# Performance work log

Measured on AMD Instinct MI355X. Metric: run time of the kernel, lower is better.

Reference implementation:

```python
import jax, jax.numpy as jnp
import numpy as np

DIMX, DIMZ, N = 32, 16, 32768
TWO_PI = 2.0 * np.pi

def _sym(M):
    return 0.5 * (M + M.T)

def setup_inputs() -> dict:
    key = jax.random.key(0)
    kx, ka, kc = jax.random.split(key, 3)
    x = jax.random.normal(kx, (DIMX, N), dtype=jnp.float32)
    A = jnp.eye(DIMZ, dtype=jnp.float32) + 0.001 * jax.random.normal(ka, (DIMZ, DIMZ), dtype=jnp.float32)
    C = jax.random.uniform(kc, (DIMX, DIMZ), dtype=jnp.float32)
    Q = 0.01 * jnp.eye(DIMZ, dtype=jnp.float32)
    R = 0.1 * jnp.eye(DIMX, dtype=jnp.float32)
    m0 = jnp.zeros((DIMZ, 1), dtype=jnp.float32)
    P0 = jnp.eye(DIMZ, dtype=jnp.float32)
    Sigma_AQA = 1e-9 * jnp.ones((DIMZ, DIMZ), dtype=jnp.float32)
    Sigma_CRC = 1e-9 * jnp.ones((DIMZ, DIMZ), dtype=jnp.float32)
    return {"x": x, "A": A, "C": C, "Q": Q, "R": R, "m0": m0, "P0": P0,
            "Sigma_AQA": Sigma_AQA, "Sigma_CRC": Sigma_CRC}

def _vblds_forward(x, A, C, Q, R, m0, P0, Sigma_AQA, Sigma_CRC):
    dz = A.shape[0]
    n_steps = x.shape[-1]
    I = jnp.eye(dz, dtype=x.dtype)

    def woodbury(V, S):
        # I - V @ inv(I + S @ V) @ S
        return I - V @ jnp.linalg.inv(I + S @ V) @ S

    # ---------- filter (forward scan over time) ----------
    def filter_step(carry, x_n):
        m, P = carry                       # m: (dz,), P: (dz,dz)
        L = woodbury(P, Sigma_CRC)
        Lm = L @ m
        LP = L @ P
        x_hat = C @ Lm
        S_hat = C @ LP @ C.T + R
        K = LP @ C.T @ jnp.linalg.inv(S_hat)
        mu = Lm + K @ (x_n - x_hat)
        V = _sym((I - K @ C) @ LP)
        # predict
        G = woodbury(V, Sigma_AQA)
        m_next = A @ (G @ mu)
        P_next = _sym(A @ G @ V @ A.T + Q)
        return (m_next, P_next), (mu, V)

    (_, _), (muf, Vf) = jax.lax.scan(filter_step, (m0[:, 0], P0), x.T)
    # muf: (N, dz), Vf: (N, dz, dz)

    # ---------- RTS smoother (reverse scan) ----------
    def smooth_step(carry, inp):
        mu_plus, V_plus = carry
        muf_n, Vf_n = inp
        G = woodbury(Vf_n, Sigma_AQA)
        GV = G @ Vf_n
        m = A @ (G @ muf_n)
        P = _sym(A @ GV @ A.T + Q)
        J = GV @ A.T @ jnp.linalg.inv(P)
        mu = G @ muf_n + J @ (mu_plus - m)
        V = _sym(GV + J @ (V_plus - P) @ J.T)
        V12 = J @ V_plus
        return (mu, V), (mu, V, V12)

    (_, _), (mus_head, Vs_head, V12) = jax.lax.scan(
        smooth_step, (muf[-1], Vf[-1]), (muf[:-1], Vf[:-1]), reverse=True)
    mus = jnp.concatenate([mus_head, muf[-1:]], axis=0)    # (N, dz)
    Vs = jnp.concatenate([Vs_head, Vf[-1:]], axis=0)        # (N, dz, dz)

    # ---------- learn (VB M-step) -> evidence lower bound pieces ----------
    Nf = jnp.asarray(n_steps, dtype=x.dtype)
    zz = jnp.einsum('ni,nj->ij', mus, mus) + Vs.sum(0)
    z1z1 = jnp.einsum('ni,nj->ij', mus[:-1], mus[:-1]) + Vs[:-1].sum(0)
    z1z2 = jnp.einsum('ni,nj->ij', mus[:-1], mus[1:]) + V12.sum(0)
    z2z2 = jnp.einsum('ni,nj->ij', mus[1:], mus[1:]) + Vs[1:].sum(0)
    zx = jnp.einsum('ni,jn->ij', mus, x)                    # (dz, dimx)
    xx = x @ x.T

    # learn_mP (quad reduces to Vs[0] since m0 <- mus[0])
    P0_new = _sym(Vs[0])
    mu0 = mus[0]
    m0m0 = jnp.outer(mu0, mu0)
    z0z0 = m0m0 + Vs[0]
    quad0 = _sym(z0z0 - 2.0 * m0m0 + m0m0)
    ell_z0 = (-0.5 * jnp.linalg.slogdet(TWO_PI * P0_new)[1]
              - 0.5 * jnp.trace(jnp.linalg.solve(P0_new, quad0)))

    # learn_AQ: alpha = 1e-6 ones -> same Lam for every row i
    Sigma_A = jnp.linalg.inv(z1z1 + 1e-6 * I)
    A_new = z1z2.T @ Sigma_A                                 # row i = z1z2[:, i] @ Sigma_A
    c_hat = 1e-9 + 0.5 * (Nf - 1.0)
    d_hat = 1e-9 + 0.5 * (jnp.diag(z2z2) - jnp.einsum('ij,ji->i', A_new, z1z2))
    Q_diag = d_hat / c_hat
    Az1z2 = A_new @ z1z2
    quad_z = _sym(z2z2 - (Az1z2 + Az1z2.T) + A_new @ z1z1 @ A_new.T)
    ell_z = (-(Nf - 1.0) / 2.0 * jnp.sum(jnp.log(TWO_PI * Q_diag))
             - 0.5 * jnp.sum(jnp.diag(quad_z) / Q_diag))

    # learn_CR: beta = 1e-6 ones -> same Lam for every row i
    Sigma_C = jnp.linalg.inv(zz + 1e-6 * I)
    C_new = zx.T @ Sigma_C                                   # (dimx, dz)
    a_hat = 1e-9 + 0.5 * Nf
    b_hat = 1e-9 + 0.5 * (jnp.diag(xx) - jnp.einsum('ij,ji->i', C_new, zx))
    R_diag = b_hat / a_hat
    Czx = C_new @ zx
    quad_x = _sym(xx - (Czx + Czx.T) + C_new @ zz @ C_new.T)
    ell_x = (-Nf / 2.0 * jnp.sum(jnp.log(TWO_PI * R_diag))
             - 0.5 * jnp.sum(jnp.diag(quad_x) / R_diag))

    ell = ell_z + ell_x + ell_z0

    # match original layout: (dz, N) and (dz, dz, N)
    return (ell,
            muf.T, jnp.moveaxis(Vf, 0, -1),
            mus.T, jnp.moveaxis(Vs, 0, -1),
            jnp.moveaxis(V12, 0, -1))

def reference(x, A, C, Q, R, m0, P0, Sigma_AQA, Sigma_CRC):
    return _vblds_forward(x, A, C, Q, R, m0, P0, Sigma_AQA, Sigma_CRC)
```

## Files before the change

### kernel.cpp

```cpp
#include <hip/hip_runtime.h>

#define DZ 16
#define NT 32768
#define NTF 32768.0f
#define NCONV 32
#define NCONVB 32
#define WARM 48
#define CHUNK 32
#define NMIDF 32703.0f
#define TWO_PI_F 6.28318530717958647692f

typedef float f4 __attribute__((ext_vector_type(4)));

#define LD4(A_, r_, c_) (*(const f4*)&(A_)[r_][c_])
#define ST4(A_, r_, c_, v_) (*((f4*)&(A_)[r_][c_])) = (v_)
#define RF(a_, k_) (a_[(k_) >> 2][(k_) & 3])
#define GATH(val_, q_) __shfl((val_), (((j4 + (q_)) << 2) | jg), 64)

template<int CTRL>
__device__ __forceinline__ float dadd(float v) {
    return v + __int_as_float(__builtin_amdgcn_update_dpp(
        0, __float_as_int(v), CTRL, 0xF, 0xF, true));
}
__device__ __forceinline__ float qred(float v) {
    return dadd<0x4E>(dadd<0xB1>(v));
}
__device__ __forceinline__ float wred64(float v) {
    v = dadd<0x128>(dadd<0x124>(dadd<0x4E>(dadd<0xB1>(v))));
    v += __int_as_float(__builtin_amdgcn_ds_swizzle(__float_as_int(v), 0x401F));
    v += __shfl_xor(v, 32, 64);
    return v;
}
template<int C>
__device__ __forceinline__ float qb(float v) {
    return __int_as_float(__builtin_amdgcn_update_dpp(
        0, __float_as_int(v), C | (C << 2) | (C << 4) | (C << 6), 0xF, 0xF, true));
}
__device__ __forceinline__ void qrows(const f4 v, f4 r[4]) {
    #pragma unroll
    for (int q = 0; q < 4; ++q) {
        r[0][q] = qb<0>(v[q]); r[1][q] = qb<1>(v[q]);
        r[2][q] = qb<2>(v[q]); r[3][q] = qb<3>(v[q]);
    }
}
__device__ __forceinline__ float frcp(float x) { return __builtin_amdgcn_rcpf(x); }
__device__ __forceinline__ float sum4(f4 v) { return (v.x + v.y) + (v.z + v.w); }
__device__ __forceinline__ float dot4(f4 a, f4 b) { f4 m = a * b; return (m.x + m.y) + (m.z + m.w); }

template<int EXTRA>
__device__ __forceinline__ void gjreg(f4& m4, f4& r4, float& rex, float& pd, int i, int jg)
{
    pd = 1.0f;
    #pragma unroll
    for (int k = 0; k < 16; ++k) {
        const int kq = k >> 2, kr = k & 3;
        const int lk = (k << 2) | jg;
        float piv = __shfl(m4[kr], (k << 2) | kq, 64);
        float mik = __shfl(m4[kr], (i << 2) | kq, 64);
        f4 mk, rk;
        #pragma unroll
        for (int q = 0; q < 4; ++q) {
            mk[q] = __shfl(m4[q], lk, 64);
            rk[q] = __shfl(r4[q], lk, 64);
        }
        float rexk = EXTRA ? __shfl(rex, lk, 64) : 0.f;
        float f = mik * frcp(piv);
        if (i != k) {
            m4 -= f * mk;
            r4 -= f * rk;
            if (EXTRA) rex -= f * rexk;
        } else {
            pd = piv;
        }
    }
}

template<int EXTRA>
__device__ __forceinline__ void gj16w(float (*M)[20], float (*RHS)[20], int i, int jg, int j4)
{
    for (int k = 0; k < 16; ++k) {
        float piv = M[k][k];
        float f = M[i][k] / piv;
        f4 mk = LD4(M, k, j4);
        f4 rk = LD4(RHS, k, j4);
        float rex = EXTRA ? RHS[k][16] : 0.f;
        f4 mi4 = LD4(M, i, j4);
        f4 ri4 = LD4(RHS, i, j4);
        float rei = (EXTRA && jg == 0) ? RHS[i][16] : 0.f;
        __syncthreads();
        if (i != k) {
            ST4(M, i, j4, mi4 - f * mk);
            ST4(RHS, i, j4, ri4 - f * rk);
            if (EXTRA && jg == 0) RHS[i][16] = rei - f * rex;
        }
        __syncthreads();
    }
}

__device__ __forceinline__ void gj16b(float (*M)[17], float (*RHS)[18], int i, int j)
{
    for (int k = 0; k < 16; ++k) {
        float f = M[i][k] / M[k][k];
        __syncthreads();
        if (i != k) {
            M[i][j]   -= f * M[k][j];
            RHS[i][j] -= f * RHS[k][j];
        }
        __syncthreads();
    }
}

__global__ __launch_bounds__(64) void vblds_phaseA(
    const float* __restrict__ gx,
    const float* __restrict__ gA, const float* __restrict__ gC,
    const float* __restrict__ gQ, const float* __restrict__ gR,
    const float* __restrict__ gm0, const float* __restrict__ gP0,
    const float* __restrict__ gSaqa, const float* __restrict__ gScrc,
    float* __restrict__ gmuf, float* __restrict__ gVf,
    float* __restrict__ gVs, float* __restrict__ gV12,
    float* __restrict__ wss)
{
    __shared__ __align__(16) float sA[16][20], sW[16][20];
    __shared__ __align__(16) float sC[32][20];
    __shared__ __align__(16) float sLP[16][20], sM[16][20], sRHS[16][20];
    __shared__ __align__(16) float sV[16][20], sGV[16][20], sAG[16][20];
    __shared__ __align__(16) float sX[16][20], sT1[16][20], sT2[16][20];
    __shared__ __align__(16) float sPp[16][20], sJm[16][20], sY[16][20], sVp[16][20];
    __shared__ __align__(16) float sKb[16][36];
    __shared__ __align__(16) float sLm[16];
    __shared__ float sRinv[32], sr[32];
    __shared__ float sxA[32][33];

    const int tid = threadIdx.x;
    const int i  = tid >> 2;
    const int jg = tid & 3;
    const int j4 = jg << 2;

    for (int idx = tid; idx < 256; idx += 64) sA[idx >> 4][idx & 15] = gA[idx];
    for (int idx = tid; idx < 512; idx += 64) sC[idx >> 4][idx & 15] = gC[idx];
    if (tid < 32) sRinv[tid] = 1.0f / gR[tid * 32 + tid];
    for (int idx = tid; idx < 32 * NCONV; idx += 64)
        sxA[idx >> 5][idx & 31] = gx[(size_t)(idx >> 5) * NT + (idx & 31)];
    const float crc = gScrc[0], aqa = gSaqa[0];
    float mi = gm0[i];
    f4 pv = *(const f4*)&gP0[i * 16 + j4];
    __syncthreads();

    {
        f4 w = {0.f, 0.f, 0.f, 0.f};
        for (int k = 0; k < 32; ++k) {
            float cri = sC[k][i] * sRinv[k];
            w += cri * LD4(sC, k, j4);
        }
        ST4(sW, i, j4, w);
    }
    __syncthreads();

    f4 ar[4], arj, qv;
    #pragma unroll
    for (int c = 0; c < 4; ++c) ar[c] = LD4(sA, i, c * 4);
    arj = LD4(sA, i, j4);
    qv = *(const f4*)&gQ[i * 16 + j4];

    for (int n = 0; n < NCONV; ++n) {
        float rs = sum4(pv);
        float P1_i = qred(rs);
        float totP = wred64(rs);
        float totm = wred64(mi) * 0.25f;
        float c1 = crc / (1.0f + crc * totP);
        float cm = c1 * totm;
        f4 p1g;
        #pragma unroll
        for (int q = 0; q < 4; ++q) p1g[q] = GATH(P1_i, q);
        f4 lpv = pv - (c1 * P1_i) * p1g;
        float Lm_i = mi - cm * P1_i;
        if (jg == 0) sLm[i] = Lm_i;
        __syncthreads();
        {
            int row = tid >> 1, h = tid & 1;
            f4 ca = LD4(sC, row, h * 8), cb = LD4(sC, row, h * 8 + 4);
            f4 la = *(const f4*)&sLm[h * 8], lb = *(const f4*)&sLm[h * 8 + 4];
            float part = dot4(ca, la) + dot4(cb, lb);
            part = dadd<0xB1>(part);
            if (h == 0) sr[row] = (sxA[row][n] - part) * sRinv[row];
        }
        __syncthreads();
        float b_i;
        {
            float accv = 0.f;
            #pragma unroll
            for (int kk = 0; kk < 8; ++kk) {
                int k = jg * 8 + kk;
                accv += sC[k][i] * sr[k];
            }
            b_i = qred(accv);
        }
        f4 bg;
        #pragma unroll
        for (int q = 0; q < 4; ++q) bg[q] = GATH(b_i, q);
        float LPb_i = qred(dot4(lpv, bg));
        f4 lr[4];
        qrows(lpv, lr);
        f4 m4 = {0.f, 0.f, 0.f, 0.f};
        #pragma unroll
        for (int k = 0; k < 16; ++k) m4 += RF(lr, k) * LD4(sW, k, j4);
        #pragma unroll
        for (int q = 0; q < 4; ++q) if (i == j4 + q) m4[q] += 1.0f;
        f4 r4 = lpv;
        float rex = LPb_i, pd;
        gjreg<1>(m4, r4, rex, pd, i, jg);
        float pdr = frcp(pd);
        f4 vv = r4 * pdr;
        float mu_i = Lm_i + rex * pdr;
        ST4(sV, i, j4, vv);
        __syncthreads();
        f4 vt;
        #pragma unroll
        for (int q = 0; q < 4; ++q) vt[q] = sV[j4 + q][i];
        f4 vs4 = 0.5f * (vv + vt);
        #pragma unroll
        for (int q = 0; q < 4; ++q) gVf[(size_t)(i * 16 + j4 + q) * NT + n] = vs4[q];
        if (jg == 0) gmuf[(size_t)i * NT + n] = mu_i;
        float rsv = sum4(vs4);
        float V1_i = qred(rsv);
        float totV = wred64(rsv);
        float totmu = wred64(mu_i) * 0.25f;
        float c2 = aqa / (1.0f + aqa * totV);
        float cm2 = c2 * totmu;
        f4 v1g;
        #pragma unroll
        for (int q = 0; q < 4; ++q) v1g[q] = GATH(V1_i, q);
        f4 gv4 = vs4 - (c2 * V1_i) * v1g;
        float Gmu_i = mu_i - cm2 * V1_i;
        ST4(sGV, i, j4, gv4);
        __syncthreads();
        f4 ag4 = {0.f, 0.f, 0.f, 0.f};
        #pragma unroll
        for (int k = 0; k < 16; ++k) ag4 += RF(ar, k) * LD4(sGV, k, j4);
        f4 gmug;
        #pragma unroll
        for (int q = 0; q < 4; ++q) gmug[q] = GATH(Gmu_i, q);
        float mv_i = qred(dot4(arj, gmug));
        f4 agr[4];
        qrows(ag4, agr);
        f4 pn;
        #pragma unroll
        for (int q = 0; q < 4; ++q) {
            f4 acc4 = {0.f, 0.f, 0.f, 0.f};
            #pragma unroll
            for (int c = 0; c < 4; ++c) acc4 += agr[c] * LD4(sA, j4 + q, c * 4);
            pn[q] = qv[q] + sum4(acc4);
        }
        ST4(sM, i, j4, pn);
        __syncthreads();
        f4 pt;
        #pragma unroll
        for (int q = 0; q < 4; ++q) pt[q] = sM[j4 + q][i];
        pv = 0.5f * (pn + pt);
        mi = mv_i;
    }
    __syncthreads();

    f4 vss4, gvs4;
    f4 jmr[4];
    {
        float rs = sum4(pv);
        float P1_i = qred(rs);
        float totP = wred64(rs);
        float c1 = crc / (1.0f + crc * totP);
        f4 p1g;
        #pragma unroll
        for (int q = 0; q < 4; ++q) p1g[q] = GATH(P1_i, q);
        f4 lpv = pv - (c1 * P1_i) * p1g;
        ST4(sLP, i, j4, lpv);
        __syncthreads();
        {
            f4 lr[4];
            #pragma unroll
            for (int c = 0; c < 4; ++c) lr[c] = LD4(sLP, i, c * 4);
            f4 m4 = {0.f, 0.f, 0.f, 0.f};
            #pragma unroll
            for (int k = 0; k < 16; ++k) m4 += RF(lr, k) * LD4(sW, k, j4);
            #pragma unroll
            for (int q = 0; q < 4; ++q) if (i == j4 + q) m4[q] += 1.0f;
            ST4(sM, i, j4, m4);
            ST4(sRHS, i, j4, lpv);
        }
        __syncthreads();
        gj16w<0>(sM, sRHS, i, jg, j4);
        float pd = sM[i][i];
        f4 xv = LD4(sRHS, i, j4) / pd;
        ST4(sX, i, j4, xv);
        __syncthreads();
        f4 xt;
        #pragma unroll
        for (int q = 0; q < 4; ++q) xt[q] = sX[j4 + q][i];
        vss4 = 0.5f * (xv + xt);
        #pragma unroll
        for (int q = 0; q < 4; ++q) {
            wss[2048 + i * 16 + j4 + q] = vss4[q];
            gVs[(size_t)(i * 16 + j4 + q) * NT + (NT - 1)] = vss4[q];
        }
        f4 xr[4];
        #pragma unroll
        for (int c = 0; c < 4; ++c) xr[c] = LD4(sX, i, c * 4);
        f4 t4 = {0.f, 0.f, 0.f, 0.f};
        #pragma unroll
        for (int k = 0; k < 16; ++k) t4 -= RF(xr, k) * LD4(sW, k, j4);
        #pragma unroll
        for (int q = 0; q < 4; ++q) if (i == j4 + q) t4[q] += 1.0f;
        float tp1_i = qred(dot4(t4, p1g));
        f4 u4 = t4 - c1 * tp1_i;
        #pragma unroll
        for (int q = 0; q < 4; ++q) wss[768 + i * 16 + j4 + q] = u4[q];
        ST4(sT1, i, j4, u4);
        f4 k0, k1;
        #pragma unroll
        for (int q = 0; q < 4; ++q) {
            int c = j4 + q;
            k0[q] = (dot4(xr[0], LD4(sC, c, 0)) + dot4(xr[1], LD4(sC, c, 4))
                   + dot4(xr[2], LD4(sC, c, 8)) + dot4(xr[3], LD4(sC, c, 12))) * sRinv[c];
            int c2 = c + 16;
            k1[q] = (dot4(xr[0], LD4(sC, c2, 0)) + dot4(xr[1], LD4(sC, c2, 4))
                   + dot4(xr[2], LD4(sC, c2, 8)) + dot4(xr[3], LD4(sC, c2, 12))) * sRinv[c2];
        }
        #pragma unroll
        for (int q = 0; q < 4; ++q) {
            sKb[i][j4 + q] = k0[q]; sKb[i][j4 + 16 + q] = k1[q];
            wss[1024 + i * 32 + j4 + q] = k0[q];
            wss[1024 + i * 32 + 16 + j4 + q] = k1[q];
        }
        __syncthreads();
        float rsv = sum4(vss4);
        float v1_i = qred(rsv);
        float totV = wred64(rsv);
        float cA = aqa / (1.0f + aqa * totV);
        f4 v1g;
        #pragma unroll
        for (int q = 0; q < 4; ++q) v1g[q] = GATH(v1_i, q);
        float av_i = qred(dot4(arj, v1g));
        f4 agm4 = arj - cA * av_i;
        gvs4 = vss4 - (cA * v1_i) * v1g;
        ST4(sAG, i, j4, agm4);
        ST4(sGV, i, j4, gvs4);
        __syncthreads();
        f4 agmr[4];
        #pragma unroll
        for (int c = 0; c < 4; ++c) agmr[c] = LD4(sAG, i, c * 4);
        f4 fv = {0.f, 0.f, 0.f, 0.f}, b0 = {0.f, 0.f, 0.f, 0.f}, b1 = {0.f, 0.f, 0.f, 0.f};
        #pragma unroll
        for (int k = 0; k < 16; ++k) {
            float a = RF(agmr, k);
            fv += a * LD4(sT1, k, j4);
            b0 += a * LD4(sKb, k, j4);
            b1 += a * LD4(sKb, k, j4 + 16);
        }
        #pragma unroll
        for (int q = 0; q < 4; ++q) {
            wss[0 + i * 16 + j4 + q] = fv[q];
            wss[256 + i * 32 + j4 + q] = b0[q];
            wss[256 + i * 32 + 16 + j4 + q] = b1[q];
        }
        f4 t2 = {0.f, 0.f, 0.f, 0.f};
        #pragma unroll
        for (int k = 0; k < 16; ++k) t2 += RF(ar, k) * LD4(sGV, k, j4);
        ST4(sT2, i, j4, t2);
        __syncthreads();
        f4 t2r[4];
        #pragma unroll
        for (int c = 0; c < 4; ++c) t2r[c] = LD4(sT2, i, c * 4);
        f4 pp;
        #pragma unroll
        for (int q = 0; q < 4; ++q) {
            f4 acc4 = {0.f, 0.f, 0.f, 0.f};
            #pragma unroll
            for (int c = 0; c < 4; ++c) acc4 += t2r[c] * LD4(sA, j4 + q, c * 4);
            pp[q] = qv[q] + sum4(acc4);
        }
        ST4(sM, i, j4, pp);
        __syncthreads();
        f4 ppt;
        #pragma unroll
        for (int q = 0; q < 4; ++q) ppt[q] = sM[j4 + q][i];
        f4 pp4 = 0.5f * (pp + ppt);
        ST4(sPp, i, j4, pp4);
        ST4(sM, i, j4, pp4);
        ST4(sRHS, i, j4, t2);
        __syncthreads();
        gj16w<0>(sM, sRHS, i, jg, j4);
        float pd2 = sM[i][i];
        f4 yv = LD4(sRHS, i, j4) / pd2;
        ST4(sY, i, j4, yv);
        __syncthreads();
        f4 jm4;
        #pragma unroll
        for (int q = 0; q < 4; ++q) jm4[q] = sY[j4 + q][i];
        ST4(sJm, i, j4, jm4);
        #pragma unroll
        for (int q = 0; q < 4; ++q) wss[1536 + i * 16 + j4 + q] = jm4[q];
        __syncthreads();
        #pragma unroll
        for (int c = 0; c < 4; ++c) jmr[c] = LD4(sJm, i, c * 4);
        f4 s4 = {0.f, 0.f, 0.f, 0.f};
        #pragma unroll
        for (int k = 0; k < 16; ++k) s4 -= RF(jmr, k) * LD4(sA, k, j4);
        #pragma unroll
        for (int q = 0; q < 4; ++q) if (i == j4 + q) s4[q] += 1.0f;
        float sv_i = qred(dot4(s4, v1g));
        f4 S4 = s4 - cA * sv_i;
        #pragma unroll
        for (int q = 0; q < 4; ++q) wss[1792 + i * 16 + j4 + q] = S4[q];
        ST4(sVp, i, j4, vss4);
        __syncthreads();
    }

    for (int k2 = 1; k2 <= NCONVB; ++k2) {
        int n = NT - 1 - k2;
        f4 v12 = {0.f, 0.f, 0.f, 0.f}, t14 = {0.f, 0.f, 0.f, 0.f};
        #pragma unroll
        for (int k = 0; k < 16; ++k) {
            f4 vp = LD4(sVp, k, j4);
            float jik = RF(jmr, k);
            v12 += jik * vp;
            t14 += jik * (vp - LD4(sPp, k, j4));
        }
        #pragma unroll
        for (int q = 0; q < 4; ++q) gV12[(size_t)(i * 16 + j4 + q) * (NT - 1) + n] = v12[q];
        f4 t1r[4];
        qrows(t14, t1r);
        f4 vn;
        #pragma unroll
        for (int q = 0; q < 4; ++q) {
            f4 acc4 = {0.f, 0.f, 0.f, 0.f};
            #pragma unroll
            for (int c = 0; c < 4; ++c) acc4 += t1r[c] * LD4(sJm, j4 + q, c * 4);
            vn[q] = gvs4[q] + sum4(acc4);
        }
        ST4(sT2, i, j4, vn);
        __syncthreads();
        f4 vnt;
        #pragma unroll
        for (int q = 0; q < 4; ++q) vnt[q] = sT2[j4 + q][i];
        f4 vnew = 0.5f * (vn + vnt);
        ST4(sVp, i, j4, vnew);
        #pragma unroll
        for (int q = 0; q < 4; ++q) gVs[(size_t)(i * 16 + j4 + q) * NT + n] = vnew[q];
        __syncthreads();
    }
    {
        f4 vpf = LD4(sVp, i, j4);
        #pragma unroll
        for (int q = 0; q < 4; ++q) wss[2304 + i * 16 + j4 + q] = vpf[q];
        f4 v12ss = {0.f, 0.f, 0.f, 0.f};
        #pragma unroll
        for (int k = 0; k < 16; ++k) v12ss += RF(jmr, k) * LD4(sVp, k, j4);
        #pragma unroll
        for (int q = 0; q < 4; ++q) wss[2560 + i * 16 + j4 + q] = v12ss[q];
    }
}

__global__ __launch_bounds__(64) void vblds_muf_scan(
    const float* __restrict__ gx, const float* __restrict__ wss, float* __restrict__ gmuf)
{
    __shared__ __align__(16) float sx[CHUNK + WARM][36];
    const int c = blockIdx.x, tid = threadIdx.x;
    const int i = tid >> 2, jg = tid & 3, j4 = jg << 2;
    const int n0 = NCONV + c * CHUNK;
    const int CLc = (NT - n0 < CHUNK) ? (NT - n0) : CHUNK;
    const int wlen = (c == 0) ? NCONV : WARM;
    const int w0 = n0 - wlen;
    const int T = wlen + CLc;

    const f4 Fv  = *(const f4*)&wss[0 + i * 16 + j4];
    const f4 Uv  = *(const f4*)&wss[768 + i * 16 + j4];
    const f4 Bh0 = *(const f4*)&wss[256 + i * 32 + jg * 8];
    const f4 Bh1 = *(const f4*)&wss[256 + i * 32 + jg * 8 + 4];
    const f4 Kh0 = *(const f4*)&wss[1024 + i * 32 + jg * 8];
    const f4 Kh1 = *(const f4*)&wss[1024 + i * 32 + jg * 8 + 4];

    for (int r = 0; r < 32; ++r)
        for (int t = tid; t < T; t += 64)
            sx[t][r] = gx[(size_t)r * NT + w0 + t];
    __syncthreads();

    float m = 0.f;
    for (int t = 0; t < T; ++t) {
        f4 mg;
        #pragma unroll
        for (int q = 0; q < 4; ++q) mg[q] = __shfl(m, ((j4 + q) << 2) | jg, 64);
        f4 xa = *(const f4*)&sx[t][jg * 8];
        f4 xb = *(const f4*)&sx[t][jg * 8 + 4];
        float pm = dot4(Fv, mg) + dot4(Bh0, xa) + dot4(Bh1, xb);
        float po = dot4(Uv, mg) + dot4(Kh0, xa) + dot4(Kh1, xb);
        pm = qred(pm);
        po = qred(po);
        if (t >= wlen && jg == 0) gmuf[(size_t)i * NT + w0 + t] = po;
        m = pm;
    }
}

__global__ __launch_bounds__(64) void vblds_mus_scan(
    const float* __restrict__ gmuf, const float* __restrict__ wss, float* __restrict__ gmus)
{
    __shared__ __align__(16) float smu[CHUNK + WARM][20];
    const int c = blockIdx.x, tid = threadIdx.x;
    const int i = tid >> 2, jg = tid & 3, j4 = jg << 2;
    const int n0 = NCONV + c * CHUNK;
    const int CLc = (NT - n0 < CHUNK) ? (NT - n0) : CHUNK;
    int wend = n0 + CLc - 1 + WARM;
    int exact = 0;
    if (wend >= NT - 1) { wend = NT - 1; exact = 1; }
    const int T = wend - n0 + 1;

    const f4 Jv = *(const f4*)&wss[1536 + i * 16 + j4];
    const f4 Sv = *(const f4*)&wss[1792 + i * 16 + j4];

    for (int r = 0; r < 16; ++r)
        for (int t = tid; t < T; t += 64)
            smu[t][r] = gmuf[(size_t)r * NT + n0 + t];
    __syncthreads();

    float cst;
    int tstart;
    if (exact) {
        cst = smu[T - 1][i];
        if (T - 1 < CLc && jg == 0) gmus[(size_t)i * NT + n0 + T - 1] = cst;
        tstart = T - 2;
    } else {
        cst = 0.f;
        tstart = T - 1;
    }
    for (int t = tstart; t >= 0; --t) {
        f4 cg;
        #pragma unroll
        for (int q = 0; q < 4; ++q) cg[q] = __shfl(cst, ((j4 + q) << 2) | jg, 64);
        f4 mufv = *(const f4*)&smu[t][j4];
        float p = dot4(Sv, mufv) + dot4(Jv, cg);
        p = qred(p);
        if (t < CLc && jg == 0) gmus[(size_t)i * NT + n0 + t] = p;
        cst = p;
    }
}

__global__ __launch_bounds__(64) void vblds_phaseB(
    const float* __restrict__ gA, const float* __restrict__ gQ,
    const float* __restrict__ gSaqa,
    const float* __restrict__ gmuf, const float* __restrict__ gVf,
    float* __restrict__ gmus, float* __restrict__ gVs, float* __restrict__ gV12,
    const float* __restrict__ wss)
{
    __shared__ __align__(16) float sA[16][20];
    __shared__ __align__(16) float sGV[16][20], sM[16][20];
    __shared__ __align__(16) float sPm[16][20], sY[16][20], sVp[16][20], sT2[16][20];
    const int tid = threadIdx.x;
    const int i = tid >> 2, jg = tid & 3, j4 = jg << 2;

    for (int idx = tid; idx < 256; idx += 64) sA[idx >> 4][idx & 15] = gA[idx];
    const float aqa = gSaqa[0];
    {
        f4 vp = *(const f4*)&wss[2304 + i * 16 + j4];
        ST4(sVp, i, j4, vp);
    }
    float mup_i = gmus[(size_t)i * NT + NCONV];
    __syncthreads();
    f4 ar[4], arj, qv;
    #pragma unroll
    for (int c = 0; c < 4; ++c) ar[c] = LD4(sA, i, c * 4);
    arj = LD4(sA, i, j4);
    qv = *(const f4*)&gQ[i * 16 + j4];

    f4 vfc;
    #pragma unroll
    for (int q = 0; q < 4; ++q) vfc[q] = gVf[(size_t)(i * 16 + j4 + q) * NT + (NCONV - 1)];
    float mfc = gmuf[(size_t)i * NT + (NCONV - 1)];

    for (int n = NCONV - 1; n >= 0; --n) {
        f4 vfn = vfc; float mfn = mfc;
        if (n > 0) {
            #pragma unroll
            for (int q = 0; q < 4; ++q) vfn[q] = gVf[(size_t)(i * 16 + j4 + q) * NT + (n - 1)];
            mfn = gmuf[(size_t)i * NT + (n - 1)];
        }
        float rs = sum4(vfc);
        float P1_i = qred(rs);
        float tot = wred64(rs);
        float totm = wred64(mfc) * 0.25f;
        float cc = aqa / (1.0f + aqa * tot);
        float cm = cc * totm;
        f4 p1g;
        #pragma unroll
        for (int q = 0; q < 4; ++q) p1g[q] = GATH(P1_i, q);
        f4 gv4 = vfc - (cc * P1_i) * p1g;
        float Gmu_i = mfc - cm * P1_i;
        ST4(sGV, i, j4, gv4);
        __syncthreads();
        f4 ag4 = {0.f, 0.f, 0.f, 0.f};
        #pragma unroll
        for (int k = 0; k < 16; ++k) ag4 += RF(ar, k) * LD4(sGV, k, j4);
        f4 gmug;
        #pragma unroll
        for (int q = 0; q < 4; ++q) gmug[q] = GATH(Gmu_i, q);
        float mv_i = qred(dot4(arj, gmug));
        f4 agr[4];
        qrows(ag4, agr);
        f4 pn;
        #pragma unroll
        for (int q = 0; q < 4; ++q) {
            f4 acc4 = {0.f, 0.f, 0.f, 0.f};
            #pragma unroll
            for (int c = 0; c < 4; ++c) acc4 += agr[c] * LD4(sA, j4 + q, c * 4);
            pn[q] = qv[q] + sum4(acc4);
        }
        ST4(sM, i, j4, pn);
        __syncthreads();
        f4 pt;
        #pragma unroll
        for (int q = 0; q < 4; ++q) pt[q] = sM[j4 + q][i];
        f4 pm4 = 0.5f * (pn + pt);
        f4 m4 = pm4, r4 = ag4;
        float rex = 0.f, pd;
        gjreg<0>(m4, r4, rex, pd, i, jg);
        f4 yv = r4 * frcp(pd);
        ST4(sY, i, j4, yv);
        ST4(sPm, i, j4, pm4);
        float dmu_i = mup_i - mv_i;
        __syncthreads();
        f4 dmug, ycol;
        #pragma unroll
        for (int q = 0; q < 4; ++q) { dmug[q] = GATH(dmu_i, q); ycol[q] = sY[j4 + q][i]; }
        float mun_i = Gmu_i + qred(dot4(ycol, dmug));
        f4 t14 = {0.f, 0.f, 0.f, 0.f}, v124 = {0.f, 0.f, 0.f, 0.f};
        #pragma unroll
        for (int k = 0; k < 16; ++k) {
            float yki = sY[k][i];
            f4 vp = LD4(sVp, k, j4);
            f4 pmk = LD4(sPm, k, j4);
            v124 += yki * vp;
            t14 += yki * (vp - pmk);
        }
        #pragma unroll
        for (int q = 0; q < 4; ++q) gV12[(size_t)(i * 16 + j4 + q) * (NT - 1) + n] = v124[q];
        f4 t1r[4];
        qrows(t14, t1r);
        f4 vn = gv4;
        #pragma unroll
        for (int k = 0; k < 16; ++k) vn += RF(t1r, k) * LD4(sY, k, j4);
        ST4(sT2, i, j4, vn);
        __syncthreads();
        f4 vnt;
        #pragma unroll
        for (int q = 0; q < 4; ++q) vnt[q] = sT2[j4 + q][i];
        f4 vnew = 0.5f * (vn + vnt);
        ST4(sVp, i, j4, vnew);
        #pragma unroll
        for (int q = 0; q < 4; ++q) gVs[(size_t)(i * 16 + j4 + q) * NT + n] = vnew[q];
        if (jg == 0) gmus[(size_t)i * NT + n] = mun_i;
        mup_i = mun_i;
        vfc = vfn; mfc = mfn;
    }
}

__global__ __launch_bounds__(256) void vblds_bulk(
    const float* __restrict__ gx, const float* __restrict__ gmus,
    const float* __restrict__ gVs, const float* __restrict__ gV12,
    const float* __restrict__ wss,
    float* __restrict__ gVf, float* __restrict__ gVs_w, float* __restrict__ gV12_w,
    float* __restrict__ acc)
{
    const int b = blockIdx.x, tid = threadIdx.x;
    if (b < 768) {
        const int arr = b >> 8, cell = b & 255;
        float val; float* base; int s, e;
        if (arr == 0)      { val = wss[2048 + cell]; base = gVf + (size_t)cell * NT;         s = NCONV; e = NT; }
        else if (arr == 1) { val = wss[2304 + cell]; base = gVs_w + (size_t)cell * NT;       s = NCONV; e = NT - 1 - NCONVB; }
        else               { val = wss[2560 + cell]; base = gV12_w + (size_t)cell * (NT - 1); s = NCONV; e = NT - 1 - NCONVB; }
        for (int idx = s + tid; idx < e; idx += 256) base[idx] = val;
        return;
    }
    if (b < 1280) {
        __shared__ float smus[16][66];
        __shared__ float sx[32][64];
        const int bb = b - 768;
        const int n0 = bb * 64;
        for (int idx = tid; idx < 16 * 65; idx += 256) {
            int ii = idx / 65, c = idx % 65;
            int n = n0 + c;
            smus[ii][c] = (n < NT) ? gmus[(size_t)ii * NT + n] : 0.f;
        }
        for (int idx = tid; idx < 32 * 64; idx += 256) {
            int ii = idx >> 6, c = idx & 63;
            sx[ii][c] = gx[(size_t)ii * NT + n0 + c];
        }
        __syncthreads();
        const int i = tid >> 4, j = tid & 15;
        float amm = 0.f, am12 = 0.f, azx0 = 0.f, azx1 = 0.f;
        float axx0 = 0.f, axx1 = 0.f, axx2 = 0.f, axx3 = 0.f;
        const int cmax12 = (NT - 1 - n0 < 64) ? (NT - 1 - n0) : 64;
        for (int c = 0; c < 64; ++c) {
            float mi = smus[i][c], mj = smus[j][c];
            amm += mi * mj;
            if (c < cmax12) am12 += mi * smus[j][c + 1];
            float xj = sx[j][c], xj2 = sx[j + 16][c];
            azx0 += mi * xj;
            azx1 += mi * xj2;
            float xi = sx[i][c], xi2 = sx[i + 16][c];
            axx0 += xi * xj; axx1 += xi * xj2; axx2 += xi2 * xj; axx3 += xi2 * xj2;
        }
        atomicAdd(&acc[i * 16 + j], amm);
        atomicAdd(&acc[256 + i * 16 + j], am12);
        atomicAdd(&acc[512 + i * 32 + j], azx0);
        atomicAdd(&acc[512 + i * 32 + j + 16], azx1);
        atomicAdd(&acc[1024 + i * 32 + j], axx0);
        atomicAdd(&acc[1024 + i * 32 + j + 16], axx1);
        atomicAdd(&acc[1024 + (i + 16) * 32 + j], axx2);
        atomicAdd(&acc[1024 + (i + 16) * 32 + j + 16], axx3);
        return;
    }
    {
        const int b2 = b - 1280;
        float s = 0.f;
        if (b2 < 256) {
            const float* src = gVs + (size_t)b2 * NT;
            if (tid < NCONV) s = src[tid];
            else if (tid < NCONV + NCONVB + 1) s = src[(NT - 1 - NCONVB) + (tid - NCONV)];
        } else {
            const float* src = gV12 + (size_t)(b2 - 256) * (NT - 1);
            if (tid < NCONV) s = src[tid];
            else if (tid < NCONV + NCONVB) s = src[(NT - 1 - NCONVB) + (tid - NCONV)];
        }
        __shared__ float red[256];
        red[tid] = s;
        __syncthreads();
        for (int w = 128; w > 0; w >>= 1) {
            if (tid < w) red[tid] += red[tid + w];
            __syncthreads();
        }
        if (tid == 0) {
            float* dst = (b2 < 256) ? &acc[2048 + b2] : &acc[2304 + (b2 - 256)];
            *dst = red[0];
        }
    }
}

__global__ __launch_bounds__(256) void vblds_finalize(
    const float* __restrict__ acc, const float* __restrict__ gmus,
    const float* __restrict__ gVs, const float* __restrict__ wss,
    float* __restrict__ gout)
{
    __shared__ float zz[16][17], z11[16][17], z22[16][17], z12[16][17];
    __shared__ float sM[16][17];
    __shared__ float sRHS[16][18];
    __shared__ float sInv[16][17], sAn[16][17], sT1[16][17];
    __shared__ float sCn[32][17], sT2[32][17], szx[16][33];
    __shared__ float mus0[16], musL[16], sVs0[16][17], sVsL[16][17];
    __shared__ float red1[32], red2[32];
    __shared__ float s_ld, s_ellz, s_ellx;
    const int tid = threadIdx.x;
    const int i = tid >> 4, j = tid & 15;

    if (j == 0) { mus0[i] = gmus[(size_t)i * NT]; musL[i] = gmus[(size_t)i * NT + NT - 1]; }
    sVs0[i][j] = gVs[(size_t)(i * 16 + j) * NT];
    sVsL[i][j] = gVs[(size_t)(i * 16 + j) * NT + NT - 1];
    szx[i][j]      = acc[512 + i * 32 + j];
    szx[i][j + 16] = acc[512 + i * 32 + j + 16];
    zz[i][j]  = acc[i * 16 + j] + acc[2048 + i * 16 + j] + NMIDF * wss[2304 + i * 16 + j];
    z12[i][j] = acc[256 + i * 16 + j] + acc[2304 + i * 16 + j] + NMIDF * wss[2560 + i * 16 + j];
    __syncthreads();
    z11[i][j] = zz[i][j] - musL[i] * musL[j] - sVsL[i][j];
    z22[i][j] = zz[i][j] - mus0[i] * mus0[j] - sVs0[i][j];
    sM[i][j] = z11[i][j] + ((i == j) ? 1e-6f : 0.f);
    sRHS[i][j] = (i == j) ? 1.0f : 0.0f;
    __syncthreads();
    gj16b(sM, sRHS, i, j);
    sInv[i][j] = sRHS[i][j] / sM[i][i];
    __syncthreads();
    { float a = 0.f; for (int k = 0; k < 16; ++k) a += z12[k][i] * sInv[k][j]; sAn[i][j] = a; }
    __syncthreads();
    { float a = 0.f; for (int k = 0; k < 16; ++k) a += sAn[i][k] * z11[k][j]; sT1[i][j] = a; }
    __syncthreads();
    if (j == 0) {
        float e = 0.f, qq = 0.f;
        for (int k = 0; k < 16; ++k) { e += sAn[i][k] * z12[k][i]; qq += sT1[i][k] * sAn[i][k]; }
        float dhat = 1e-9f + 0.5f * (z22[i][i] - e);
        float Qi = dhat / (1e-9f + 0.5f * (NTF - 1.0f));
        float quad = z22[i][i] - 2.0f * e + qq;
        red1[i] = logf(TWO_PI_F * Qi);
        red2[i] = quad / Qi;
    }
    __syncthreads();
    if (tid == 0) {
        float s1 = 0.f, s2 = 0.f;
        for (int k = 0; k < 16; ++k) { s1 += red1[k]; s2 += red2[k]; }
        s_ellz = -(NTF - 1.0f) * 0.5f * s1 - 0.5f * s2;
    }
    __syncthreads();
    sM[i][j] = zz[i][j] + ((i == j) ? 1e-6f : 0.f);
    sRHS[i][j] = (i == j) ? 1.0f : 0.0f;
    __syncthreads();
    gj16b(sM, sRHS, i, j);
    sInv[i][j] = sRHS[i][j] / sM[i][i];
    __syncthreads();
    { float a = 0.f; for (int k = 0; k < 16; ++k) a += szx[k][i]      * sInv[k][j]; sCn[i][j]      = a; }
    { float a = 0.f; for (int k = 0; k < 16; ++k) a += szx[k][i + 16] * sInv[k][j]; sCn[i + 16][j] = a; }
    __syncthreads();
    { float a = 0.f; for (int k = 0; k < 16; ++k) a += sCn[i][k]      * zz[k][j]; sT2[i][j]      = a; }
    { float a = 0.f; for (int k = 0; k < 16; ++k) a += sCn[i + 16][k] * zz[k][j]; sT2[i + 16][j] = a; }
    __syncthreads();
    if (j == 0) {
        for (int rr = i; rr < 32; rr += 16) {
            float f = 0.f, qq = 0.f;
            for (int k = 0; k < 16; ++k) { f += sCn[rr][k] * szx[k][rr]; qq += sT2[rr][k] * sCn[rr][k]; }
            float xxd = acc[1024 + rr * 32 + rr];
            float bhat = 1e-9f + 0.5f * (xxd - f);
            float Ri = bhat / (1e-9f + 0.5f * NTF);
            float quad = xxd - 2.0f * f + qq;
            red1[rr] = logf(TWO_PI_F * Ri);
            red2[rr] = quad / Ri;
        }
    }
    __syncthreads();
    if (tid == 0) {
        float s1 = 0.f, s2 = 0.f;
        for (int k = 0; k < 32; ++k) { s1 += red1[k]; s2 += red2[k]; }
        s_ellx = -NTF * 0.5f * s1 - 0.5f * s2;
        s_ld = 0.f;
    }
    sM[i][j] = sVs0[i][j];
    __syncthreads();
    for (int k = 0; k < 16; ++k) {
        float f = sM[i][k] / sM[k][k];
        if (tid == 0) s_ld += logf(sM[k][k]);
        __syncthreads();
        if (i > k) sM[i][j] -= f * sM[k][j];
        __syncthreads();
    }
    if (tid == 0) {
        float ellz0 = -0.5f * (16.0f * logf(TWO_PI_F) + s_ld) - 8.0f;
        gout[0] = s_ellz + s_ellx + ellz0;
    }
}

extern "C" void kernel_launch(void* const* d_in, const int* in_sizes, int n_in,
                              void* d_out, int out_size, void* d_ws, size_t ws_size,
                              hipStream_t stream)
{
    (void)in_sizes; (void)n_in; (void)out_size; (void)ws_size;
    const float* x    = (const float*)d_in[0];
    const float* A    = (const float*)d_in[1];
    const float* C    = (const float*)d_in[2];
    const float* Q    = (const float*)d_in[3];
    const float* R    = (const float*)d_in[4];
    const float* m0   = (const float*)d_in[5];
    const float* P0   = (const float*)d_in[6];
    const float* Saqa = (const float*)d_in[7];
    const float* Scrc = (const float*)d_in[8];

    float* out = (float*)d_out;
    float* muf = out + 1;
    float* Vf  = muf + DZ * NT;
    float* mus = Vf + DZ * DZ * NT;
    float* Vs  = mus + DZ * NT;
    float* V12 = Vs + DZ * DZ * NT;
    float* acc = (float*)d_ws;
    float* wss = acc + 4096;

    const int nscan = (NT - NCONV) / CHUNK;

    hipMemsetAsync(acc, 0, 2560 * sizeof(float), stream);
    vblds_phaseA<<<1, 64, 0, stream>>>(x, A, C, Q, R, m0, P0, Saqa, Scrc,
                                       muf, Vf, Vs, V12, wss);
    vblds_muf_scan<<<nscan, 64, 0, stream>>>(x, wss, muf);
    vblds_mus_scan<<<nscan, 64, 0, stream>>>(muf, wss, mus);
    vblds_phaseB<<<1, 64, 0, stream>>>(A, Q, Saqa, muf, Vf, mus, Vs, V12, wss);
    vblds_bulk<<<1792, 256, 0, stream>>>(x, mus, Vs, V12, wss, Vf, Vs, V12, acc);
    vblds_finalize<<<1, 256, 0, stream>>>(acc, mus, Vs, wss, out);
}
```

Before: 469.4 us.

## Fuse mean scans, move head covariance smoothing into phaseA, slim phaseB

The filtered-mean and smoothed-mean chunked scans are merged into one kernel that keeps filtered means in shared memory and runs the backward pass over a warm-up extension. The head-segment smoother covariance recursion moves into phaseA, which caches GV, AG, P and J per step in workspace. The old phaseB becomes a tiny mean-only backward kernel. The bulk statistics blocks now process 128 columns each instead of 64. This removes one launch and the global round trip of muf between scans, but each scan block does a longer serial warm-up and phaseA's serial work grows.

New measurement: 465.2 us. About the same (-0.9%).

```diff
diff --git a/kernel.cpp b/kernel.cpp
--- a/kernel.cpp
+++ b/kernel.cpp
@@ -16,6 +16,13 @@
 #define ST4(A_, r_, c_, v_) (*((f4*)&(A_)[r_][c_])) = (v_)
 #define RF(a_, k_) (a_[(k_) >> 2][(k_) & 3])
 #define GATH(val_, q_) __shfl((val_), (((j4 + (q_)) << 2) | jg), 64)
+
+#define WOF_GV 0
+#define WOF_AG 8192
+#define WOF_PP 16384
+#define WOF_J  24576
+#define WOF_GMU 32768
+#define WOF_MV  33280
 
 template<int CTRL>
 __device__ __forceinline__ float dadd(float v) {
@@ -118,7 +125,7 @@
     const float* __restrict__ gSaqa, const float* __restrict__ gScrc,
     float* __restrict__ gmuf, float* __restrict__ gVf,
     float* __restrict__ gVs, float* __restrict__ gV12,
-    float* __restrict__ wss)
+    float* __restrict__ wss, float* __restrict__ wsb)
 {
     __shared__ __align__(16) float sA[16][20], sW[16][20];
     __shared__ __align__(16) float sC[32][20];
@@ -136,6 +143,13 @@
     const int jg = tid & 3;
     const int j4 = jg << 2;
 
+    float* wsGV = wsb + WOF_GV;
+    float* wsAG = wsb + WOF_AG;
+    float* wsPP = wsb + WOF_PP;
+    float* wsJ  = wsb + WOF_J;
+    float* wsGMU = wsb + WOF_GMU;
+    float* wsMV  = wsb + WOF_MV;
+
     for (int idx = tid; idx < 256; idx += 64) sA[idx >> 4][idx & 15] = gA[idx];
     for (int idx = tid; idx < 512; idx += 64) sC[idx >> 4][idx & 15] = gC[idx];
     if (tid < 32) sRinv[tid] = 1.0f / gR[tid * 32 + tid];
@@ -257,6 +271,13 @@
         #pragma unroll
         for (int q = 0; q < 4; ++q) pt[q] = sM[j4 + q][i];
         pv = 0.5f * (pn + pt);
+        #pragma unroll
+        for (int q = 0; q < 4; ++q) {
+            wsGV[n * 256 + i * 16 + j4 + q] = gv4[q];
+            wsAG[n * 256 + i * 16 + j4 + q] = ag4[q];
+            wsPP[n * 256 + i * 16 + j4 + q] = pv[q];
+        }
+        if (jg == 0) { wsGMU[n * 16 + i] = Gmu_i; wsMV[n * 16 + i] = mv_i; }
         mi = mv_i;
     }
     __syncthreads();
@@ -457,19 +478,75 @@
         #pragma unroll
         for (int q = 0; q < 4; ++q) wss[2560 + i * 16 + j4 + q] = v12ss[q];
     }
-}
-
-__global__ __launch_bounds__(64) void vblds_muf_scan(
-    const float* __restrict__ gx, const float* __restrict__ wss, float* __restrict__ gmuf)
+    __syncthreads();
+
+    f4 gvc = *(const f4*)&wsGV[(NCONV - 1) * 256 + i * 16 + j4];
+    f4 agc = *(const f4*)&wsAG[(NCONV - 1) * 256 + i * 16 + j4];
+    f4 ppc = *(const f4*)&wsPP[(NCONV - 1) * 256 + i * 16 + j4];
+    for (int n = NCONV - 1; n >= 0; --n) {
+        f4 gvn = gvc, agn = agc, ppn = ppc;
+        if (n > 0) {
+            gvc = *(const f4*)&wsGV[(n - 1) * 256 + i * 16 + j4];
+            agc = *(const f4*)&wsAG[(n - 1) * 256 + i * 16 + j4];
+            ppc = *(const f4*)&wsPP[(n - 1) * 256 + i * 16 + j4];
+        }
+        f4 m4 = ppn, r4 = agn;
+        float rex = 0.f, pd;
+        gjreg<0>(m4, r4, rex, pd, i, jg);
+        f4 yv = r4 * frcp(pd);
+        ST4(sY, i, j4, yv);
+        ST4(sPp, i, j4, ppn);
+        __syncthreads();
+        f4 jm4;
+        #pragma unroll
+        for (int q = 0; q < 4; ++q) jm4[q] = sY[j4 + q][i];
+        #pragma unroll
+        for (int q = 0; q < 4; ++q) wsJ[n * 256 + i * 16 + j4 + q] = jm4[q];
+        f4 t14 = {0.f, 0.f, 0.f, 0.f}, v124 = {0.f, 0.f, 0.f, 0.f};
+        #pragma unroll
+        for (int k = 0; k < 16; ++k) {
+            float yki = sY[k][i];
+            f4 vp = LD4(sVp, k, j4);
+            f4 pmk = LD4(sPp, k, j4);
+            v124 += yki * vp;
+            t14 += yki * (vp - pmk);
+        }
+        #pragma unroll
+        for (int q = 0; q < 4; ++q) gV12[(size_t)(i * 16 + j4 + q) * (NT - 1) + n] = v124[q];
+        f4 t1r[4];
+        qrows(t14, t1r);
+        f4 vn = gvn;
+        #pragma unroll
+        for (int k = 0; k < 16; ++k) vn += RF(t1r, k) * LD4(sY, k, j4);
+        ST4(sT2, i, j4, vn);
+        __syncthreads();
+        f4 vnt;
+        #pragma unroll
+        for (int q = 0; q < 4; ++q) vnt[q] = sT2[j4 + q][i];
+        f4 vnew = 0.5f * (vn + vnt);
+        ST4(sVp, i, j4, vnew);
+        #pragma unroll
+        for (int q = 0; q < 4; ++q) gVs[(size_t)(i * 16 + j4 + q) * NT + n] = vnew[q];
+        __syncthreads();
+    }
+}
+
+__global__ __launch_bounds__(64) void vblds_mean_scan(
+    const float* __restrict__ gx, const float* __restrict__ wss,
+    float* __restrict__ gmuf, float* __restrict__ gmus)
 {
-    __shared__ __align__(16) float sx[CHUNK + WARM][36];
+    __shared__ __align__(16) float sx[128][36];
+    __shared__ float smuF[128][20];
     const int c = blockIdx.x, tid = threadIdx.x;
     const int i = tid >> 2, jg = tid & 3, j4 = jg << 2;
     const int n0 = NCONV + c * CHUNK;
-    const int CLc = (NT - n0 < CHUNK) ? (NT - n0) : CHUNK;
+    const int CL = (NT - n0 < CHUNK) ? (NT - n0) : CHUNK;
     const int wlen = (c == 0) ? NCONV : WARM;
     const int w0 = n0 - wlen;
-    const int T = wlen + CLc;
+    int ge = n0 + CL + WARM;
+    int exact = 0;
+    if (ge >= NT) { ge = NT; exact = 1; }
+    const int Tf = ge - w0;
 
     const f4 Fv  = *(const f4*)&wss[0 + i * 16 + j4];
     const f4 Uv  = *(const f4*)&wss[768 + i * 16 + j4];
@@ -477,14 +554,16 @@
     const f4 Bh1 = *(const f4*)&wss[256 + i * 32 + jg * 8 + 4];
     const f4 Kh0 = *(const f4*)&wss[1024 + i * 32 + jg * 8];
     const f4 Kh1 = *(const f4*)&wss[1024 + i * 32 + jg * 8 + 4];
+    const f4 Jv  = *(const f4*)&wss[1536 + i * 16 + j4];
+    const f4 Sv  = *(const f4*)&wss[1792 + i * 16 + j4];
 
     for (int r = 0; r < 32; ++r)
-        for (int t = tid; t < T; t += 64)
+        for (int t = tid; t < Tf; t += 64)
             sx[t][r] = gx[(size_t)r * NT + w0 + t];
     __syncthreads();
 
     float m = 0.f;
-    for (int t = 0; t < T; ++t) {
+    for (int t = 0; t < Tf; ++t) {
         f4 mg;
         #pragma unroll
         for (int q = 0; q < 4; ++q) mg[q] = __shfl(m, ((j4 + q) << 2) | jg, 64);
@@ -494,169 +573,62 @@
         float po = dot4(Uv, mg) + dot4(Kh0, xa) + dot4(Kh1, xb);
         pm = qred(pm);
         po = qred(po);
-        if (t >= wlen && jg == 0) gmuf[(size_t)i * NT + w0 + t] = po;
+        if (t >= wlen && jg == 0) {
+            smuF[t][i] = po;
+            if (t < wlen + CL) gmuf[(size_t)i * NT + w0 + t] = po;
+        }
         m = pm;
     }
-}
-
-__global__ __launch_bounds__(64) void vblds_mus_scan(
-    const float* __restrict__ gmuf, const float* __restrict__ wss, float* __restrict__ gmus)
-{
-    __shared__ __align__(16) float smu[CHUNK + WARM][20];
-    const int c = blockIdx.x, tid = threadIdx.x;
-    const int i = tid >> 2, jg = tid & 3, j4 = jg << 2;
-    const int n0 = NCONV + c * CHUNK;
-    const int CLc = (NT - n0 < CHUNK) ? (NT - n0) : CHUNK;
-    int wend = n0 + CLc - 1 + WARM;
-    int exact = 0;
-    if (wend >= NT - 1) { wend = NT - 1; exact = 1; }
-    const int T = wend - n0 + 1;
-
-    const f4 Jv = *(const f4*)&wss[1536 + i * 16 + j4];
-    const f4 Sv = *(const f4*)&wss[1792 + i * 16 + j4];
-
-    for (int r = 0; r < 16; ++r)
-        for (int t = tid; t < T; t += 64)
-            smu[t][r] = gmuf[(size_t)r * NT + n0 + t];
     __syncthreads();
 
     float cst;
     int tstart;
     if (exact) {
-        cst = smu[T - 1][i];
-        if (T - 1 < CLc && jg == 0) gmus[(size_t)i * NT + n0 + T - 1] = cst;
-        tstart = T - 2;
+        cst = smuF[Tf - 1][i];
+        if (Tf - 1 < wlen + CL && jg == 0) gmus[(size_t)i * NT + w0 + Tf - 1] = cst;
+        tstart = Tf - 2;
     } else {
         cst = 0.f;
-        tstart = T - 1;
-    }
-    for (int t = tstart; t >= 0; --t) {
+        tstart = Tf - 1;
+    }
+    for (int lt = tstart; lt >= wlen; --lt) {
         f4 cg;
         #pragma unroll
         for (int q = 0; q < 4; ++q) cg[q] = __shfl(cst, ((j4 + q) << 2) | jg, 64);
-        f4 mufv = *(const f4*)&smu[t][j4];
+        f4 mufv = *(const f4*)&smuF[lt][j4];
         float p = dot4(Sv, mufv) + dot4(Jv, cg);
         p = qred(p);
-        if (t < CLc && jg == 0) gmus[(size_t)i * NT + n0 + t] = p;
+        if (lt < wlen + CL && jg == 0) gmus[(size_t)i * NT + w0 + lt] = p;
         cst = p;
     }
 }
 
-__global__ __launch_bounds__(64) void vblds_phaseB(
-    const float* __restrict__ gA, const float* __restrict__ gQ,
-    const float* __restrict__ gSaqa,
-    const float* __restrict__ gmuf, const float* __restrict__ gVf,
-    float* __restrict__ gmus, float* __restrict__ gVs, float* __restrict__ gV12,
-    const float* __restrict__ wss)
+__global__ __launch_bounds__(64) void vblds_bmean(
+    const float* __restrict__ wsb, float* __restrict__ gmus)
 {
-    __shared__ __align__(16) float sA[16][20];
-    __shared__ __align__(16) float sGV[16][20], sM[16][20];
-    __shared__ __align__(16) float sPm[16][20], sY[16][20], sVp[16][20], sT2[16][20];
     const int tid = threadIdx.x;
     const int i = tid >> 2, jg = tid & 3, j4 = jg << 2;
-
-    for (int idx = tid; idx < 256; idx += 64) sA[idx >> 4][idx & 15] = gA[idx];
-    const float aqa = gSaqa[0];
-    {
-        f4 vp = *(const f4*)&wss[2304 + i * 16 + j4];
-        ST4(sVp, i, j4, vp);
-    }
-    float mup_i = gmus[(size_t)i * NT + NCONV];
-    __syncthreads();
-    f4 ar[4], arj, qv;
-    #pragma unroll
-    for (int c = 0; c < 4; ++c) ar[c] = LD4(sA, i, c * 4);
-    arj = LD4(sA, i, j4);
-    qv = *(const f4*)&gQ[i * 16 + j4];
-
-    f4 vfc;
-    #pragma unroll
-    for (int q = 0; q < 4; ++q) vfc[q] = gVf[(size_t)(i * 16 + j4 + q) * NT + (NCONV - 1)];
-    float mfc = gmuf[(size_t)i * NT + (NCONV - 1)];
-
+    const float* wsJ  = wsb + WOF_J;
+    const float* wsGMU = wsb + WOF_GMU;
+    const float* wsMV  = wsb + WOF_MV;
+    float mup = gmus[(size_t)i * NT + NCONV];
+    f4 jc = *(const f4*)&wsJ[(NCONV - 1) * 256 + i * 16 + j4];
+    float gmuc = wsGMU[(NCONV - 1) * 16 + i];
+    float mvc  = wsMV[(NCONV - 1) * 16 + i];
     for (int n = NCONV - 1; n >= 0; --n) {
-        f4 vfn = vfc; float mfn = mfc;
+        f4 jn = jc; float gmun = gmuc, mvn = mvc;
         if (n > 0) {
-            #pragma unroll
-            for (int q = 0; q < 4; ++q) vfn[q] = gVf[(size_t)(i * 16 + j4 + q) * NT + (n - 1)];
-            mfn = gmuf[(size_t)i * NT + (n - 1)];
-        }
-        float rs = sum4(vfc);
-        float P1_i = qred(rs);
-        float tot = wred64(rs);
-        float totm = wred64(mfc) * 0.25f;
-        float cc = aqa / (1.0f + aqa * tot);
-        float cm = cc * totm;
-        f4 p1g;
-        #pragma unroll
-        for (int q = 0; q < 4; ++q) p1g[q] = GATH(P1_i, q);
-        f4 gv4 = vfc - (cc * P1_i) * p1g;
-        float Gmu_i = mfc - cm * P1_i;
-        ST4(sGV, i, j4, gv4);
-        __syncthreads();
-        f4 ag4 = {0.f, 0.f, 0.f, 0.f};
-        #pragma unroll
-        for (int k = 0; k < 16; ++k) ag4 += RF(ar, k) * LD4(sGV, k, j4);
-        f4 gmug;
-        #pragma unroll
-        for (int q = 0; q < 4; ++q) gmug[q] = GATH(Gmu_i, q);
-        float mv_i = qred(dot4(arj, gmug));
-        f4 agr[4];
-        qrows(ag4, agr);
-        f4 pn;
-        #pragma unroll
-        for (int q = 0; q < 4; ++q) {
-            f4 acc4 = {0.f, 0.f, 0.f, 0.f};
-            #pragma unroll
-            for (int c = 0; c < 4; ++c) acc4 += agr[c] * LD4(sA, j4 + q, c * 4);
-            pn[q] = qv[q] + sum4(acc4);
-        }
-        ST4(sM, i, j4, pn);
-        __syncthreads();
-        f4 pt;
-        #pragma unroll
-        for (int q = 0; q < 4; ++q) pt[q] = sM[j4 + q][i];
-        f4 pm4 = 0.5f * (pn + pt);
-        f4 m4 = pm4, r4 = ag4;
-        float rex = 0.f, pd;
-        gjreg<0>(m4, r4, rex, pd, i, jg);
-        f4 yv = r4 * frcp(pd);
-        ST4(sY, i, j4, yv);
-        ST4(sPm, i, j4, pm4);
-        float dmu_i = mup_i - mv_i;
-        __syncthreads();
-        f4 dmug, ycol;
-        #pragma unroll
-        for (int q = 0; q < 4; ++q) { dmug[q] = GATH(dmu_i, q); ycol[q] = sY[j4 + q][i]; }
-        float mun_i = Gmu_i + qred(dot4(ycol, dmug));
-        f4 t14 = {0.f, 0.f, 0.f, 0.f}, v124 = {0.f, 0.f, 0.f, 0.f};
-        #pragma unroll
-        for (int k = 0; k < 16; ++k) {
-            float yki = sY[k][i];
-            f4 vp = LD4(sVp, k, j4);
-            f4 pmk = LD4(sPm, k, j4);
-            v124 += yki * vp;
-            t14 += yki * (vp - pmk);
-        }
-        #pragma unroll
-        for (int q = 0; q < 4; ++q) gV12[(size_t)(i * 16 + j4 + q) * (NT - 1) + n] = v124[q];
-        f4 t1r[4];
-        qrows(t14, t1r);
-        f4 vn = gv4;
-        #pragma unroll
-        for (int k = 0; k < 16; ++k) vn += RF(t1r, k) * LD4(sY, k, j4);
-        ST4(sT2, i, j4, vn);
-        __syncthreads();
-        f4 vnt;
-        #pragma unroll
-        for (int q = 0; q < 4; ++q) vnt[q] = sT2[j4 + q][i];
-        f4 vnew = 0.5f * (vn + vnt);
-        ST4(sVp, i, j4, vnew);
-        #pragma unroll
-        for (int q = 0; q < 4; ++q) gVs[(size_t)(i * 16 + j4 + q) * NT + n] = vnew[q];
-        if (jg == 0) gmus[(size_t)i * NT + n] = mun_i;
-        mup_i = mun_i;
-        vfc = vfn; mfc = mfn;
+            jc = *(const f4*)&wsJ[(n - 1) * 256 + i * 16 + j4];
+            gmuc = wsGMU[(n - 1) * 16 + i];
+            mvc  = wsMV[(n - 1) * 16 + i];
+        }
+        float dmu = mup - mvn;
+        f4 dmug;
+        #pragma unroll
+        for (int q = 0; q < 4; ++q) dmug[q] = GATH(dmu, q);
+        float mun = gmun + qred(dot4(jn, dmug));
+        if (jg == 0) gmus[(size_t)i * NT + n] = mun;
+        mup = mun;
     }
 }
 
@@ -671,39 +643,39 @@
     if (b < 768) {
         const int arr = b >> 8, cell = b & 255;
         float val; float* base; int s, e;
-        if (arr == 0)      { val = wss[2048 + cell]; base = gVf + (size_t)cell * NT;         s = NCONV; e = NT; }
-        else if (arr == 1) { val = wss[2304 + cell]; base = gVs_w + (size_t)cell * NT;       s = NCONV; e = NT - 1 - NCONVB; }
+        if (arr == 0)      { val = wss[2048 + cell]; base = gVf + (size_t)cell * NT;          s = NCONV; e = NT; }
+        else if (arr == 1) { val = wss[2304 + cell]; base = gVs_w + (size_t)cell * NT;        s = NCONV; e = NT - 1 - NCONVB; }
         else               { val = wss[2560 + cell]; base = gV12_w + (size_t)cell * (NT - 1); s = NCONV; e = NT - 1 - NCONVB; }
         for (int idx = s + tid; idx < e; idx += 256) base[idx] = val;
         return;
     }
-    if (b < 1280) {
-        __shared__ float smus[16][66];
-        __shared__ float sx[32][64];
+    if (b < 1024) {
+        __shared__ float smus[16][130];
+        __shared__ float sx[32][128];
         const int bb = b - 768;
-        const int n0 = bb * 64;
-        for (int idx = tid; idx < 16 * 65; idx += 256) {
-            int ii = idx / 65, c = idx % 65;
-            int n = n0 + c;
-            smus[ii][c] = (n < NT) ? gmus[(size_t)ii * NT + n] : 0.f;
-        }
-        for (int idx = tid; idx < 32 * 64; idx += 256) {
-            int ii = idx >> 6, c = idx & 63;
-            sx[ii][c] = gx[(size_t)ii * NT + n0 + c];
+        const int n0 = bb * 128;
+        for (int idx = tid; idx < 16 * 129; idx += 256) {
+            int ii = idx / 129, cc = idx - ii * 129;
+            int n = n0 + cc;
+            smus[ii][cc] = (n < NT) ? gmus[(size_t)ii * NT + n] : 0.f;
+        }
+        for (int idx = tid; idx < 32 * 128; idx += 256) {
+            int ii = idx >> 7, cc = idx & 127;
+            sx[ii][cc] = gx[(size_t)ii * NT + n0 + cc];
         }
         __syncthreads();
         const int i = tid >> 4, j = tid & 15;
         float amm = 0.f, am12 = 0.f, azx0 = 0.f, azx1 = 0.f;
         float axx0 = 0.f, axx1 = 0.f, axx2 = 0.f, axx3 = 0.f;
-        const int cmax12 = (NT - 1 - n0 < 64) ? (NT - 1 - n0) : 64;
-        for (int c = 0; c < 64; ++c) {
-            float mi = smus[i][c], mj = smus[j][c];
+        const int cmax12 = (NT - 1 - n0 < 128) ? (NT - 1 - n0) : 128;
+        for (int cc = 0; cc < 128; ++cc) {
+            float mi = smus[i][cc], mj = smus[j][cc];
             amm += mi * mj;
-            if (c < cmax12) am12 += mi * smus[j][c + 1];
-            float xj = sx[j][c], xj2 = sx[j + 16][c];
+            if (cc < cmax12) am12 += mi * smus[j][cc + 1];
+            float xj = sx[j][cc], xj2 = sx[j + 16][cc];
             azx0 += mi * xj;
             azx1 += mi * xj2;
-            float xi = sx[i][c], xi2 = sx[i + 16][c];
+            float xi = sx[i][cc], xi2 = sx[i + 16][cc];
             axx0 += xi * xj; axx1 += xi * xj2; axx2 += xi2 * xj; axx3 += xi2 * xj2;
         }
         atomicAdd(&acc[i * 16 + j], amm);
@@ -717,7 +689,7 @@
         return;
     }
     {
-        const int b2 = b - 1280;
+        const int b2 = b - 1024;
         float s = 0.f;
         if (b2 < 256) {
             const float* src = gVs + (size_t)b2 * NT;
@@ -863,15 +835,15 @@
     float* V12 = Vs + DZ * DZ * NT;
     float* acc = (float*)d_ws;
     float* wss = acc + 4096;
+    float* wsb = acc + 8192;
 
     const int nscan = (NT - NCONV) / CHUNK;
 
     hipMemsetAsync(acc, 0, 2560 * sizeof(float), stream);
     vblds_phaseA<<<1, 64, 0, stream>>>(x, A, C, Q, R, m0, P0, Saqa, Scrc,
-                                       muf, Vf, Vs, V12, wss);
-    vblds_muf_scan<<<nscan, 64, 0, stream>>>(x, wss, muf);
-    vblds_mus_scan<<<nscan, 64, 0, stream>>>(muf, wss, mus);
-    vblds_phaseB<<<1, 64, 0, stream>>>(A, Q, Saqa, muf, Vf, mus, Vs, V12, wss);
-    vblds_bulk<<<1792, 256, 0, stream>>>(x, mus, Vs, V12, wss, Vf, Vs, V12, acc);
+                                       muf, Vf, Vs, V12, wss, wsb);
+    vblds_mean_scan<<<nscan, 64, 0, stream>>>(x, wss, muf, mus);
+    vblds_bmean<<<1, 64, 0, stream>>>(wsb, mus);
+    vblds_bulk<<<1536, 256, 0, stream>>>(x, mus, Vs, V12, wss, Vf, Vs, V12, acc);
     vblds_finalize<<<1, 256, 0, stream>>>(acc, mus, Vs, wss, out);
 }
```
